# Optimization experiments

Hardware: AMD Instinct MI355X
Metric: run time of the kernel (lower is better)

Reference implementation:

```python
import jax, jax.numpy as jnp
import numpy as np

K_NEIGHBORS = 5
LEAKY_SLOPE = 0.2
NEG_INF = -1e9


def create_knn(x, k):
    # x: [B, N, D] -> binary adjacency [B, N, N], adj[b,i,j]=1 if j is among
    # the k nearest neighbors of i (squared euclidean distance).
    sq = jnp.sum(x * x, axis=-1)                      # [B, N]
    # d2[b,i,j] = |xi|^2 + |xj|^2 - 2 xi.xj
    d2 = sq[:, :, None] + sq[:, None, :] - 2.0 * jnp.einsum('bid,bjd->bij', x, x)
    _, idx = jax.lax.top_k(-d2, k)                    # [B, N, k] nearest (incl. self)
    B, N, _ = x.shape
    b_idx = jnp.arange(B)[:, None, None]
    i_idx = jnp.arange(N)[None, :, None]
    adj = jnp.zeros((B, N, N), dtype=x.dtype).at[b_idx, i_idx, idx].set(1.0)
    return adj


def gat_layer(x, adj, W, a_src, a_dst):
    # Single-head GAT over dense kNN adjacency.
    h = jnp.einsum('bnd,df->bnf', x, W)               # [B, N, F]
    e_src = jnp.einsum('bnf,f->bn', h, a_src)         # [B, N]
    e_dst = jnp.einsum('bnf,f->bn', h, a_dst)         # [B, N]
    e = e_src[:, :, None] + e_dst[:, None, :]         # [B, N, N]
    e = jax.nn.leaky_relu(e, negative_slope=LEAKY_SLOPE)
    e = jnp.where(adj > 0, e, NEG_INF)
    alpha = jax.nn.softmax(e, axis=-1)                # [B, N, N]
    out = jnp.einsum('bij,bjf->bif', alpha, h)        # [B, N, F]
    return jax.nn.elu(out)


def setup_inputs() -> dict:
    key = jax.random.key(0)
    k1, k2, k3, k4 = jax.random.split(key, 4)
    B, N, D = 256, 196, 2048
    F = D // 4
    return {
        'resnet_features': jax.random.normal(k1, (B, N, D), dtype=jnp.float32),
        'W': jax.random.normal(k2, (D, F), dtype=jnp.float32) * (1.0 / np.sqrt(D)),
        'a_src': jax.random.normal(k3, (F,), dtype=jnp.float32) * (1.0 / np.sqrt(F)),
        'a_dst': jax.random.normal(k4, (F,), dtype=jnp.float32) * (1.0 / np.sqrt(F)),
    }


def reference(resnet_features, W, a_src, a_dst):
    adj = create_knn(resnet_features, K_NEIGHBORS)
    return gat_layer(resnet_features, adj, W, a_src, a_dst)
```

## Files before the change

### kernel.cpp

```cpp
#include <hip/hip_runtime.h>

#define B_  256
#define N_  196
#define D_  2048
#define F_  512
#define ROWS (B_*N_)
#define CAND 8
#define PROWS 208
#define PELEMS (PROWS*32)

typedef _Float16 f16x8 __attribute__((ext_vector_type(8)));
typedef _Float16 f16x4 __attribute__((ext_vector_type(4)));
typedef float    f32x4 __attribute__((ext_vector_type(4)));

static __device__ __forceinline__ float wave_reduce_sum(float v) {
#pragma unroll
  for (int off = 32; off > 0; off >>= 1) v += __shfl_xor(v, off);
  return v;
}

static __device__ __forceinline__ double wave_reduce_sum_d(double v) {
#pragma unroll
  for (int off = 32; off > 0; off >>= 1) v += __shfl_xor(v, off);
  return v;
}

static __device__ __forceinline__ float np_chain16(const float* __restrict__ x, int h) {
  int base = (h >> 3) * 128 + (h & 7);
  float t0 = x[base];
  float r = __fmul_rn(t0, t0);
#pragma unroll
  for (int i = 1; i < 16; ++i) {
    float t = x[base + 8 * i];
    r = __fadd_rn(r, __fmul_rn(t, t));
  }
  return r;
}
static __device__ __forceinline__ float np_sq_row(const float* __restrict__ x, int lane) {
  float ra = np_chain16(x, lane);
  float rb = np_chain16(x, lane + 64);
#pragma unroll
  for (int off = 1; off <= 4; off <<= 1) {
    ra = __fadd_rn(ra, __shfl_xor(ra, off));
    rb = __fadd_rn(rb, __shfl_xor(rb, off));
  }
  float lf[16];
#pragma unroll
  for (int L = 0; L < 8; ++L) { lf[L] = __shfl(ra, L * 8); lf[8 + L] = __shfl(rb, L * 8); }
  float b8[8];
#pragma unroll
  for (int t = 0; t < 8; ++t) b8[t] = __fadd_rn(lf[2 * t], lf[2 * t + 1]);
  float c4[4];
#pragma unroll
  for (int t = 0; t < 4; ++t) c4[t] = __fadd_rn(b8[2 * t], b8[2 * t + 1]);
  return __fadd_rn(__fadd_rn(c4[0], c4[1]), __fadd_rn(c4[2], c4[3]));
}

__global__ __launch_bounds__(256) void wtrans_kernel(const float* __restrict__ W,
                                                     _Float16* __restrict__ Wt2) {
  __shared__ float T[64][68];
  int k0 = blockIdx.x * 64;
  int f0 = blockIdx.y * 64;
  int tid = threadIdx.x;
  int c = tid & 63;
  int r4 = tid >> 6;
#pragma unroll
  for (int p = 0; p < 16; ++p) {
    int r = p * 4 + r4;
    T[r][c] = W[(size_t)(k0 + r) * F_ + f0 + c];
  }
  __syncthreads();
#pragma unroll
  for (int p = 0; p < 16; ++p) {
    int fr = p * 4 + r4;
    int kg = k0 + c;
    Wt2[(size_t)(kg >> 5) * F_ * 32 + (size_t)(f0 + fr) * 32 + (kg & 31)] = (_Float16)T[c][fr];
  }
}

__global__ __launch_bounds__(256, 3) void h_gemm(const float* __restrict__ X,
                                                 const _Float16* __restrict__ Wt2,
                                                 float* __restrict__ H) {
  __shared__ _Float16 Al[2][64][40];
  const int mBase = blockIdx.y * 64;
  const int nBase = blockIdx.x * 256;
  const int tid  = threadIdx.x;
  const int lane = tid & 63;
  const int wave = tid >> 6;
  const int fr_row = lane & 15;
  const int fr_k   = (lane >> 4) * 8;
  const int ar = tid >> 2;
  const int ak = (tid & 3) * 8;
  f32x4 acc[4][4] = {};

  const _Float16* Bb = Wt2 + (size_t)(nBase + wave * 64 + fr_row) * 32 + fr_k;
  const size_t PSTRIDE = (size_t)F_ * 32;

  f16x8 bf[4];
#pragma unroll
  for (int n = 0; n < 4; ++n) bf[n] = *(const f16x8*)&Bb[(size_t)n * 512];

  {
    float4 a0 = *(const float4*)&X[(size_t)(mBase + ar) * D_ + ak];
    float4 a1 = *(const float4*)&X[(size_t)(mBase + ar) * D_ + ak + 4];
    f16x8 ah = { (_Float16)a0.x, (_Float16)a0.y, (_Float16)a0.z, (_Float16)a0.w,
                 (_Float16)a1.x, (_Float16)a1.y, (_Float16)a1.z, (_Float16)a1.w };
    *(f16x8*)&Al[0][ar][ak] = ah;
  }
  __syncthreads();

  for (int t = 0; t < 64; ++t) {
    const int cur = t & 1;
    float4 na0, na1; f16x8 nb[4];
    if (t < 63) {
      const int k0 = (t + 1) * 32;
      na0 = *(const float4*)&X[(size_t)(mBase + ar) * D_ + k0 + ak];
      na1 = *(const float4*)&X[(size_t)(mBase + ar) * D_ + k0 + ak + 4];
      const _Float16* bp = Bb + (size_t)(t + 1) * PSTRIDE;
#pragma unroll
      for (int n = 0; n < 4; ++n) nb[n] = *(const f16x8*)&bp[(size_t)n * 512];
    }
    f16x8 af[4];
#pragma unroll
    for (int m = 0; m < 4; ++m) af[m] = *(const f16x8*)&Al[cur][m * 16 + fr_row][fr_k];
#pragma unroll
    for (int m = 0; m < 4; ++m)
#pragma unroll
      for (int n = 0; n < 4; ++n)
        acc[m][n] = __builtin_amdgcn_mfma_f32_16x16x32_f16(af[m], bf[n], acc[m][n], 0, 0, 0);
    if (t < 63) {
      f16x8 ah = { (_Float16)na0.x, (_Float16)na0.y, (_Float16)na0.z, (_Float16)na0.w,
                   (_Float16)na1.x, (_Float16)na1.y, (_Float16)na1.z, (_Float16)na1.w };
      *(f16x8*)&Al[cur ^ 1][ar][ak] = ah;
#pragma unroll
      for (int n = 0; n < 4; ++n) bf[n] = nb[n];
    }
    __syncthreads();
  }

  const int orow0 = mBase + (lane >> 4) * 4;
#pragma unroll
  for (int m = 0; m < 4; ++m) {
#pragma unroll
    for (int n = 0; n < 4; ++n) {
      int col = nBase + wave * 64 + n * 16 + (lane & 15);
#pragma unroll
      for (int i = 0; i < 4; ++i)
        H[(size_t)(orow0 + m * 16 + i) * F_ + col] = acc[m][n][i];
    }
  }
}

__global__ __launch_bounds__(512, 2) void h_gemm_pan(const float* __restrict__ X,
                                                     const _Float16* __restrict__ Wt2,
                                                     const float* __restrict__ As,
                                                     const float* __restrict__ Ad,
                                                     float* __restrict__ H,
                                                     _Float16* __restrict__ Xh,
                                                     float* __restrict__ sqg,
                                                     float* __restrict__ es,
                                                     float* __restrict__ ed) {
  __shared__ _Float16 Al[2][64][40];
  __shared__ float eS[64][8];
  __shared__ float eD[64][8];
  const int mBase = blockIdx.x * 64;
  const int tid  = threadIdx.x;
  const int lane = tid & 63;
  const int wave = tid >> 6;
  const int fr_row = lane & 15;
  const int fr_k   = (lane >> 4) * 8;
  const int ar = tid >> 3;
  const int ak = (tid & 7) * 4;
  f32x4 acc[4][4] = {};
  float sqp = 0.f;

  const int grow = mBase + ar;
  const int bb = grow / N_;
  const int rl = grow - bb * N_;
  _Float16* pRow = Xh + (size_t)bb * 64 * PELEMS + (size_t)rl * 32 + ak;

  const _Float16* Bb = Wt2 + (size_t)(wave * 64 + fr_row) * 32 + fr_k;
  const size_t PSTRIDE = (size_t)F_ * 32;

  f16x8 bf[4];
#pragma unroll
  for (int n = 0; n < 4; ++n) bf[n] = *(const f16x8*)&Bb[(size_t)n * 512];

  {
    float4 a0 = *(const float4*)&X[(size_t)grow * D_ + ak];
    f16x4 ah = { (_Float16)a0.x, (_Float16)a0.y, (_Float16)a0.z, (_Float16)a0.w };
    *(f16x4*)&Al[0][ar][ak] = ah;
    sqp += a0.x * a0.x + a0.y * a0.y + a0.z * a0.z + a0.w * a0.w;
    *(f16x4*)pRow = ah;
  }
  __syncthreads();

  for (int t = 0; t < 64; ++t) {
    const int cur = t & 1;
    float4 na; f16x8 nb[4];
    if (t < 63) {
      const int k0 = (t + 1) * 32;
      na = *(const float4*)&X[(size_t)grow * D_ + k0 + ak];
      const _Float16* bp = Bb + (size_t)(t + 1) * PSTRIDE;
#pragma unroll
      for (int n = 0; n < 4; ++n) nb[n] = *(const f16x8*)&bp[(size_t)n * 512];
    }
    f16x8 af[4];
#pragma unroll
    for (int m = 0; m < 4; ++m) af[m] = *(const f16x8*)&Al[cur][m * 16 + fr_row][fr_k];
#pragma unroll
    for (int m = 0; m < 4; ++m)
#pragma unroll
      for (int n = 0; n < 4; ++n)
        acc[m][n] = __builtin_amdgcn_mfma_f32_16x16x32_f16(af[m], bf[n], acc[m][n], 0, 0, 0);
    if (t < 63) {
      f16x4 nah = { (_Float16)na.x, (_Float16)na.y, (_Float16)na.z, (_Float16)na.w };
      *(f16x4*)&Al[cur ^ 1][ar][ak] = nah;
      sqp += na.x * na.x + na.y * na.y + na.z * na.z + na.w * na.w;
      *(f16x4*)(pRow + (size_t)(t + 1) * PELEMS) = nah;
#pragma unroll
      for (int n = 0; n < 4; ++n) bf[n] = nb[n];
    }
    __syncthreads();
  }

  {
    float s = sqp;
    s += __shfl_xor(s, 1); s += __shfl_xor(s, 2); s += __shfl_xor(s, 4);
    if ((lane & 7) == 0) sqg[grow] = s;
  }

  {
    float as_v[4], ad_v[4];
#pragma unroll
    for (int n = 0; n < 4; ++n) {
      int col = wave * 64 + n * 16 + (lane & 15);
      as_v[n] = As[col]; ad_v[n] = Ad[col];
    }
#pragma unroll
    for (int m = 0; m < 4; ++m) {
#pragma unroll
      for (int i = 0; i < 4; ++i) {
        float ps = 0.f, pd = 0.f;
#pragma unroll
        for (int n = 0; n < 4; ++n) {
          ps += acc[m][n][i] * as_v[n];
          pd += acc[m][n][i] * ad_v[n];
        }
#pragma unroll
        for (int off = 1; off <= 8; off <<= 1) {
          ps += __shfl_xor(ps, off);
          pd += __shfl_xor(pd, off);
        }
        if ((lane & 15) == 0) {
          int row_loc = (lane >> 4) * 4 + i + m * 16;
          eS[row_loc][wave] = ps;
          eD[row_loc][wave] = pd;
        }
      }
    }
  }
  __syncthreads();
  if (tid < 64) {
    float s = 0.f, d = 0.f;
#pragma unroll
    for (int w = 0; w < 8; ++w) { s += eS[tid][w]; d += eD[tid][w]; }
    es[mBase + tid] = s;
    ed[mBase + tid] = d;
  }

  const int orow0 = mBase + (lane >> 4) * 4;
#pragma unroll
  for (int m = 0; m < 4; ++m) {
#pragma unroll
    for (int n = 0; n < 4; ++n) {
      int col = wave * 64 + n * 16 + (lane & 15);
#pragma unroll
      for (int i = 0; i < 4; ++i)
        H[(size_t)(orow0 + m * 16 + i) * F_ + col] = acc[m][n][i];
    }
  }
}

__global__ __launch_bounds__(256) void e_kernel(const float* __restrict__ H,
                                                const float* __restrict__ as,
                                                const float* __restrict__ ad,
                                                float* __restrict__ es,
                                                float* __restrict__ ed) {
  int row  = blockIdx.x * 4 + (threadIdx.x >> 6);
  int lane = threadIdx.x & 63;
  const float* h = H + (size_t)row * F_;
  float s = 0.f, d = 0.f;
#pragma unroll
  for (int p = 0; p < 2; ++p) {
    int col = p * 256 + lane * 4;
    float4 hv = *(const float4*)&h[col];
    float4 av = *(const float4*)&as[col];
    float4 dv = *(const float4*)&ad[col];
    s += hv.x * av.x + hv.y * av.y + hv.z * av.z + hv.w * av.w;
    d += hv.x * dv.x + hv.y * dv.y + hv.z * dv.z + hv.w * dv.w;
  }
  s = wave_reduce_sum(s);
  d = wave_reduce_sum(d);
  if (lane == 0) { es[row] = s; ed[row] = d; }
}

__global__ __launch_bounds__(256, 3) void knn_screen(const float* __restrict__ X,
                                                     int* __restrict__ cand8,
                                                     float* __restrict__ gapw) {
  __shared__ _Float16 T[2][256][40];
  __shared__ float sqA[256];

  const int bi  = blockIdx.x;
  const int xcd = bi & 7;
  const int kk  = bi >> 3;
  const int b   = ((kk >> 2) << 3) | xcd;
  const int i0  = (kk & 3) * 64;

  const int tid  = threadIdx.x;
  const int lane = tid & 63;
  const int wave = tid >> 6;
  const float* Xb = X + (size_t)b * N_ * D_;
  const int fr_row = lane & 15;
  const int fr_k   = (lane >> 4) * 8;
  const int srow = tid >> 3;
  const int skk  = (tid & 7) * 4;

  f32x4 acc[13] = {};
  float sqp[8] = {};

  {
    float4 v[8];
#pragma unroll
    for (int p = 0; p < 8; ++p) {
      int r = p * 32 + srow;
      v[p] = make_float4(0.f, 0.f, 0.f, 0.f);
      if (r < N_) v[p] = *(const float4*)&Xb[(size_t)r * D_ + skk];
    }
#pragma unroll
    for (int p = 0; p < 8; ++p) {
      int r = p * 32 + srow;
      sqp[p] += v[p].x * v[p].x + v[p].y * v[p].y + v[p].z * v[p].z + v[p].w * v[p].w;
      f16x4 h4 = { (_Float16)v[p].x, (_Float16)v[p].y, (_Float16)v[p].z, (_Float16)v[p].w };
      *(f16x4*)&T[0][r][skk] = h4;
    }
  }
  __syncthreads();

  for (int t = 0; t < 64; ++t) {
    const int cur = t & 1;
    float4 nv[8];
    if (t < 63) {
      const int k0 = (t + 1) * 32;
#pragma unroll
      for (int p = 0; p < 8; ++p) {
        int r = p * 32 + srow;
        nv[p] = make_float4(0.f, 0.f, 0.f, 0.f);
        if (r < N_) nv[p] = *(const float4*)&Xb[(size_t)r * D_ + k0 + skk];
      }
    }
    f16x8 a0 = *(const f16x8*)&T[cur][i0 + wave * 16 + fr_row][fr_k];
#pragma unroll
    for (int n = 0; n < 13; ++n) {
      f16x8 bfr = *(const f16x8*)&T[cur][n * 16 + fr_row][fr_k];
      acc[n] = __builtin_amdgcn_mfma_f32_16x16x32_f16(a0, bfr, acc[n], 0, 0, 0);
    }
    if (t < 63) {
#pragma unroll
      for (int p = 0; p < 8; ++p) {
        int r = p * 32 + srow;
        sqp[p] += nv[p].x * nv[p].x + nv[p].y * nv[p].y + nv[p].z * nv[p].z + nv[p].w * nv[p].w;
        f16x4 h4 = { (_Float16)nv[p].x, (_Float16)nv[p].y, (_Float16)nv[p].z, (_Float16)nv[p].w };
        *(f16x4*)&T[cur ^ 1][r][skk] = h4;
      }
    }
    __syncthreads();
  }

#pragma unroll
  for (int p = 0; p < 8; ++p) {
    float s = sqp[p];
    s += __shfl_xor(s, 1); s += __shfl_xor(s, 2); s += __shfl_xor(s, 4);
    if ((lane & 7) == 0) sqA[p * 32 + srow] = s;
  }
  __syncthreads();

  float sqv[13];
#pragma unroll
  for (int n = 0; n < 13; ++n) sqv[n] = sqA[n * 16 + (lane & 15)];
  const int g = lane >> 4;
#pragma unroll
  for (int i = 0; i < 4; ++i) {
    int row_loc = wave * 16 + g * 4 + i;
    float w13[13];
#pragma unroll
    for (int n = 0; n < 13; ++n) {
      int col = n * 16 + (lane & 15);
      w13[n] = (col < N_) ? (sqv[n] - 2.0f * acc[n][i]) : 1e30f;
    }
    int candv[CAND]; float mscv[CAND];
#pragma unroll
    for (int it = 0; it < CAND; ++it) {
      float mv = w13[0]; int mn = 0;
#pragma unroll
      for (int n = 1; n < 13; ++n)
        if (w13[n] < mv) { mv = w13[n]; mn = n; }
      int mcol = mn * 16 + (lane & 15);
#pragma unroll
      for (int off = 1; off <= 8; off <<= 1) {
        float ov = __shfl_xor(mv, off);
        int   oc = __shfl_xor(mcol, off);
        if (ov < mv || (ov == mv && oc < mcol)) { mv = ov; mcol = oc; }
      }
      mscv[it] = mv; candv[it] = mcol;
      int kn = mcol >> 4;
#pragma unroll
      for (int n = 0; n < 13; ++n)
        if (n == kn && (lane & 15) == (mcol & 15)) w13[n] = 1e30f;
    }
    int ig = i0 + row_loc;
    if ((lane & 15) == 0 && ig < N_) {
      size_t o = ((size_t)b * N_ + ig) * CAND;
#pragma unroll
      for (int c = 0; c < CAND; ++c) cand8[o + c] = candv[c];
      gapw[b * N_ + ig] = mscv[5] - mscv[4];
    }
  }
}

__global__ __launch_bounds__(256) void knn_screen_pan(const _Float16* __restrict__ Xh,
                                                      const float* __restrict__ sqg,
                                                      int* __restrict__ cand8,
                                                      float* __restrict__ gapw) {
  const int bi  = blockIdx.x;
  const int xcd = bi & 7;
  const int kk  = bi >> 3;
  const int b   = ((kk >> 2) << 3) | xcd;
  const int i0  = (kk & 3) * 64;

  const int tid  = threadIdx.x;
  const int lane = tid & 63;
  const int wave = tid >> 6;
  if (i0 + wave * 16 >= N_) return;

  const int fr_row = lane & 15;
  const int fr_k   = (lane >> 4) * 8;

  const _Float16* Pb = Xh + (size_t)b * 64 * PELEMS;
  const int aoff = (i0 + wave * 16 + fr_row) * 32 + fr_k;

  f32x4 acc[13] = {};
#pragma unroll 2
  for (int t = 0; t < 64; ++t) {
    const _Float16* P = Pb + (size_t)t * PELEMS;
    f16x8 a0 = *(const f16x8*)&P[aoff];
#pragma unroll
    for (int n = 0; n < 13; ++n) {
      f16x8 bfr = *(const f16x8*)&P[(n * 16 + fr_row) * 32 + fr_k];
      acc[n] = __builtin_amdgcn_mfma_f32_16x16x32_f16(a0, bfr, acc[n], 0, 0, 0);
    }
  }

  float sqv[13];
#pragma unroll
  for (int n = 0; n < 13; ++n) {
    int col = n * 16 + (lane & 15);
    sqv[n] = (col < N_) ? sqg[b * N_ + col] : 0.f;
  }
  const int g = lane >> 4;
#pragma unroll
  for (int i = 0; i < 4; ++i) {
    int row_loc = wave * 16 + g * 4 + i;
    float w13[13];
#pragma unroll
    for (int n = 0; n < 13; ++n) {
      int col = n * 16 + (lane & 15);
      w13[n] = (col < N_) ? (sqv[n] - 2.0f * acc[n][i]) : 1e30f;
    }
    int candv[CAND]; float mscv[CAND];
#pragma unroll
    for (int it = 0; it < CAND; ++it) {
      float mv = w13[0]; int mn = 0;
#pragma unroll
      for (int n = 1; n < 13; ++n)
        if (w13[n] < mv) { mv = w13[n]; mn = n; }
      int mcol = mn * 16 + (lane & 15);
#pragma unroll
      for (int off = 1; off <= 8; off <<= 1) {
        float ov = __shfl_xor(mv, off);
        int   oc = __shfl_xor(mcol, off);
        if (ov < mv || (ov == mv && oc < mcol)) { mv = ov; mcol = oc; }
      }
      mscv[it] = mv; candv[it] = mcol;
      int kn = mcol >> 4;
#pragma unroll
      for (int n = 0; n < 13; ++n)
        if (n == kn && (lane & 15) == (mcol & 15)) w13[n] = 1e30f;
    }
    int ig = i0 + row_loc;
    if ((lane & 15) == 0 && ig < N_) {
      size_t o = ((size_t)b * N_ + ig) * CAND;
#pragma unroll
      for (int c = 0; c < CAND; ++c) cand8[o + c] = candv[c];
      gapw[b * N_ + ig] = mscv[5] - mscv[4];
    }
  }
}

__global__ __launch_bounds__(256) void knn_resolve(const float* __restrict__ X,
                                                   const int* __restrict__ cand8,
                                                   const float* __restrict__ gapw,
                                                   const float* __restrict__ es,
                                                   const float* __restrict__ ed,
                                                   int* __restrict__ idx5,
                                                   float* __restrict__ alpha5) {
  const int gr   = blockIdx.x * 4 + (threadIdx.x >> 6);
  const int lane = threadIdx.x & 63;
  const int b    = gr / N_;
  const int ig   = gr - b * N_;
  const float* Xb = X + (size_t)b * N_ * D_;
  const float* xi = Xb + (size_t)ig * D_;

  int cand[CAND];
#pragma unroll
  for (int c = 0; c < CAND; ++c) cand[c] = cand8[(size_t)gr * CAND + c];
  float gap = gapw[gr];

  int ordj[5];
  if (gap > 0.75f) {
#pragma unroll
    for (int m5 = 0; m5 < 5; ++m5) ordj[m5] = cand[m5];
  } else {
    float4 xr[8];
#pragma unroll
    for (int q = 0; q < 8; ++q) xr[q] = *(const float4*)&xi[q * 256 + lane * 4];
    double s8[CAND];
#pragma unroll
    for (int c = 0; c < CAND; ++c) {
      const float* xj = Xb + (size_t)cand[c] * D_;
      double dsum = 0.0, sqc = 0.0;
#pragma unroll
      for (int q = 0; q < 8; ++q) {
        float4 u = *(const float4*)&xj[q * 256 + lane * 4];
        dsum += (double)xr[q].x * (double)u.x + (double)xr[q].y * (double)u.y
              + (double)xr[q].z * (double)u.z + (double)xr[q].w * (double)u.w;
        sqc  += (double)u.x * (double)u.x + (double)u.y * (double)u.y
              + (double)u.z * (double)u.z + (double)u.w * (double)u.w;
      }
      dsum = wave_reduce_sum_d(dsum);
      sqc  = wave_reduce_sum_d(sqc);
      s8[c] = sqc - 2.0 * dsum;
    }
    int rnk[CAND];
#pragma unroll
    for (int c = 0; c < CAND; ++c) {
      int r = 0;
#pragma unroll
      for (int c2 = 0; c2 < CAND; ++c2)
        if (c2 != c && (s8[c2] < s8[c] || (s8[c2] == s8[c] && cand[c2] < cand[c]))) r++;
      rnk[c] = r;
    }
    double g5 = 0.0, g6 = 0.0;
#pragma unroll
    for (int c = 0; c < CAND; ++c) {
      if (rnk[c] == 4) g5 = s8[c];
      if (rnk[c] == 5) g6 = s8[c];
    }
#pragma unroll
    for (int m5 = 0; m5 < 5; ++m5) {
      int oj = 0;
#pragma unroll
      for (int c = 0; c < CAND; ++c)
        if (rnk[c] == m5) oj = cand[c];
      ordj[m5] = oj;
    }
    if (!(g6 - g5 > 4e-3)) {
      float sqi_ex = np_sq_row(xi, lane);
      float sqc_ex[CAND];
#pragma unroll
      for (int c = 0; c < CAND; ++c)
        sqc_ex[c] = np_sq_row(Xb + (size_t)cand[c] * D_, lane);
      int grp8 = (lane >> 2) & 7;
      int l4 = lane & 3;
      int cj = cand[0];
#pragma unroll
      for (int c = 1; c < CAND; ++c)
        if (grp8 == c) cj = cand[c];
      const float* xjr = Xb + (size_t)cj * D_;
      float aacc = 0.f;
      for (int s5 = 0; s5 < 512; ++s5) {
        int d = s5 * 4 + l4;
        aacc = __fadd_rn(aacc, __fmul_rn(xi[d], xjr[d]));
      }
      float d2c[CAND];
#pragma unroll
      for (int c = 0; c < CAND; ++c) {
        float s0 = __shfl(aacc, c * 4 + 0);
        float s1 = __shfl(aacc, c * 4 + 1);
        float s2 = __shfl(aacc, c * 4 + 2);
        float s3 = __shfl(aacc, c * 4 + 3);
        float G  = __fadd_rn(__fadd_rn(s0, s1), __fadd_rn(s2, s3));
        float Sij = __fadd_rn(sqi_ex, sqc_ex[c]);
        d2c[c] = __fsub_rn(Sij, __fadd_rn(G, G));
      }
      int rnk3[CAND];
#pragma unroll
      for (int c = 0; c < CAND; ++c) {
        int r = 0;
#pragma unroll
        for (int c2 = 0; c2 < CAND; ++c2)
          if (c2 != c && (d2c[c2] < d2c[c] || (d2c[c2] == d2c[c] && cand[c2] < cand[c]))) r++;
        rnk3[c] = r;
      }
#pragma unroll
      for (int m5 = 0; m5 < 5; ++m5) {
        int oj = 0;
#pragma unroll
        for (int c = 0; c < CAND; ++c)
          if (rnk3[c] == m5) oj = cand[c];
        ordj[m5] = oj;
      }
    }
  }
  float ei = es[gr];
  float ev[5];
#pragma unroll
  for (int m5 = 0; m5 < 5; ++m5) {
    float e = ei + ed[b * N_ + ordj[m5]];
    ev[m5] = e > 0.f ? e : 0.2f * e;
  }
  float mx = fmaxf(fmaxf(fmaxf(ev[0], ev[1]), fmaxf(ev[2], ev[3])), ev[4]);
  float p0 = expf(ev[0] - mx), p1 = expf(ev[1] - mx), p2 = expf(ev[2] - mx),
        p3 = expf(ev[3] - mx), p4 = expf(ev[4] - mx);
  float inv = 1.0f / (p0 + p1 + p2 + p3 + p4);
  if (lane == 0) {
    size_t o = (size_t)gr * 5;
    idx5[o + 0] = ordj[0]; alpha5[o + 0] = p0 * inv;
    idx5[o + 1] = ordj[1]; alpha5[o + 1] = p1 * inv;
    idx5[o + 2] = ordj[2]; alpha5[o + 2] = p2 * inv;
    idx5[o + 3] = ordj[3]; alpha5[o + 3] = p3 * inv;
    idx5[o + 4] = ordj[4]; alpha5[o + 4] = p4 * inv;
  }
}

__global__ __launch_bounds__(128) void agg_kernel(const float* __restrict__ H,
                                                  const int* __restrict__ idx5,
                                                  const float* __restrict__ alpha5,
                                                  float* __restrict__ out) {
  int row = blockIdx.x;
  int b = row / N_;
  int t = threadIdx.x;
  size_t base5 = (size_t)row * 5;
  const float* Hb = H + (size_t)b * N_ * F_;
  float ax = 0.f, ay = 0.f, az = 0.f, aw = 0.f;
#pragma unroll
  for (int c = 0; c < 5; ++c) {
    int j   = idx5[base5 + c];
    float a = alpha5[base5 + c];
    float4 hv = *(const float4*)&Hb[(size_t)j * F_ + t * 4];
    ax += a * hv.x; ay += a * hv.y; az += a * hv.z; aw += a * hv.w;
  }
  float4 o;
  o.x = ax > 0.f ? ax : expf(ax) - 1.f;
  o.y = ay > 0.f ? ay : expf(ay) - 1.f;
  o.z = az > 0.f ? az : expf(az) - 1.f;
  o.w = aw > 0.f ? aw : expf(aw) - 1.f;
  *(float4*)&out[(size_t)row * F_ + t * 4] = o;
}

extern "C" void kernel_launch(void* const* d_in, const int* in_sizes, int n_in,
                              void* d_out, int out_size, void* d_ws, size_t ws_size,
                              hipStream_t stream) {
  const float* X    = (const float*)d_in[0];
  const float* W    = (const float*)d_in[1];
  const float* Asrc = (const float*)d_in[2];
  const float* Adst = (const float*)d_in[3];
  float* out = (float*)d_out;

  const size_t OFF_WT  = 0;
  const size_t OFF_ES  = OFF_WT + 2097152;
  const size_t OFF_ED  = OFF_ES + 200704;
  const size_t OFF_IDX = OFF_ED + 200704;
  const size_t OFF_ALP = OFF_IDX + 1003520;
  const size_t OFF_C8  = OFF_ALP + 1003520;
  const size_t OFF_GAP = OFF_C8 + 1605632;
  const size_t OFF_SQG = OFF_GAP + 200704;
  const size_t OFF_H   = OFF_SQG + 200704;
  const size_t OFF_XH  = OFF_H + (size_t)ROWS * F_ * 4;
  const size_t XH_BYTES = (size_t)B_ * 64 * PELEMS * 2;
  const size_t NEED_A  = OFF_XH;
  const size_t NEED_B  = OFF_XH + XH_BYTES;
  if (ws_size < NEED_A) return;

  char* ws = (char*)d_ws;
  _Float16* Wt2 = (_Float16*)(ws + OFF_WT);
  float* es     = (float*)(ws + OFF_ES);
  float* ed     = (float*)(ws + OFF_ED);
  int*   idx5   = (int*)  (ws + OFF_IDX);
  float* alpha5 = (float*)(ws + OFF_ALP);
  int*   cand8  = (int*)  (ws + OFF_C8);
  float* gapw   = (float*)(ws + OFF_GAP);
  float* sqg    = (float*)(ws + OFF_SQG);
  float* H      = (float*)(ws + OFF_H);
  _Float16* Xh  = (_Float16*)(ws + OFF_XH);

  wtrans_kernel<<<dim3(32, 8), 256, 0, stream>>>(W, Wt2);
  if (ws_size >= NEED_B) {
    h_gemm_pan<<<784, 512, 0, stream>>>(X, Wt2, Asrc, Adst, H, Xh, sqg, es, ed);
    knn_screen_pan<<<1024, 256, 0, stream>>>(Xh, sqg, cand8, gapw);
  } else {
    h_gemm<<<dim3(2, 784), 256, 0, stream>>>(X, Wt2, H);
    e_kernel<<<ROWS / 4, 256, 0, stream>>>(H, Asrc, Adst, es, ed);
    knn_screen<<<1024, 256, 0, stream>>>(X, cand8, gapw);
  }
  knn_resolve<<<ROWS / 4, 256, 0, stream>>>(X, cand8, gapw, es, ed, idx5, alpha5);
  agg_kernel<<<ROWS, 128, 0, stream>>>(H, idx5, alpha5, out);
}
```

Before: 684.9 us.

## Split fp32-to-fp16 panelization from GEMM and feed MFMA directly from panels

The fused GEMM that both converted X to fp16 panels and computed H is split in two. A separate panelize kernel writes the fp16 panels and row norms, and a new 2-way N-split GEMM loads A fragments straight from the panel buffer in global memory, with no LDS staging or barriers. Attention logit partial sums are written per N half and combined in knn_resolve. This adds an extra pass writing the fp16 copy of X, and A panels are re-read by both N halves, in exchange for a simpler, barrier-free GEMM inner loop with more blocks.

```diff
diff --git a/kernel.cpp b/kernel.cpp
--- a/kernel.cpp
+++ b/kernel.cpp
@@ -75,6 +75,127 @@
     int fr = p * 4 + r4;
     int kg = k0 + c;
     Wt2[(size_t)(kg >> 5) * F_ * 32 + (size_t)(f0 + fr) * 32 + (kg & 31)] = (_Float16)T[c][fr];
+  }
+}
+
+__global__ __launch_bounds__(256) void panelize_kernel(const float* __restrict__ X,
+                                                       _Float16* __restrict__ Xh,
+                                                       float* __restrict__ sqg) {
+  const int tid = threadIdx.x;
+  const int ar  = tid >> 3;
+  const int ak  = (tid & 7) * 4;
+  const int lane = tid & 63;
+  const int grow = blockIdx.x * 32 + ar;
+  const int bb = grow / N_;
+  const int rl = grow - bb * N_;
+  const float* xr = X + (size_t)grow * D_;
+  _Float16* pRow = Xh + (size_t)bb * 64 * PELEMS + (size_t)rl * 32 + ak;
+  float sqp = 0.f;
+#pragma unroll 4
+  for (int t = 0; t < 64; ++t) {
+    float4 v = *(const float4*)&xr[t * 32 + ak];
+    sqp += v.x * v.x + v.y * v.y + v.z * v.z + v.w * v.w;
+    f16x4 h4 = { (_Float16)v.x, (_Float16)v.y, (_Float16)v.z, (_Float16)v.w };
+    *(f16x4*)(pRow + (size_t)t * PELEMS) = h4;
+  }
+  sqp += __shfl_xor(sqp, 1); sqp += __shfl_xor(sqp, 2); sqp += __shfl_xor(sqp, 4);
+  if ((lane & 7) == 0) sqg[grow] = sqp;
+}
+
+__global__ __launch_bounds__(256) void h_gemm_p(const _Float16* __restrict__ Xh,
+                                                const _Float16* __restrict__ Wt2,
+                                                const float* __restrict__ As,
+                                                const float* __restrict__ Ad,
+                                                float* __restrict__ H,
+                                                float* __restrict__ esp,
+                                                float* __restrict__ edp) {
+  __shared__ float eS[64][4];
+  __shared__ float eD[64][4];
+  const int mBase = blockIdx.y * 64;
+  const int half  = blockIdx.x;
+  const int nBase = half * 256;
+  const int tid  = threadIdx.x;
+  const int lane = tid & 63;
+  const int wave = tid >> 6;
+  const int fr_row = lane & 15;
+  const int fr_k   = (lane >> 4) * 8;
+  f32x4 acc[4][4] = {};
+
+  const _Float16* pA[4];
+#pragma unroll
+  for (int m = 0; m < 4; ++m) {
+    int rg = mBase + m * 16 + fr_row;
+    int bb = rg / N_;
+    int rl = rg - bb * N_;
+    pA[m] = Xh + (size_t)bb * 64 * PELEMS + (size_t)rl * 32 + fr_k;
+  }
+  const _Float16* Bb = Wt2 + (size_t)(nBase + wave * 64 + fr_row) * 32 + fr_k;
+  const size_t PSTRIDE = (size_t)F_ * 32;
+
+#pragma unroll 2
+  for (int t = 0; t < 64; ++t) {
+    const size_t po = (size_t)t * PELEMS;
+    const _Float16* bp = Bb + (size_t)t * PSTRIDE;
+    f16x8 af[4], bf[4];
+#pragma unroll
+    for (int m = 0; m < 4; ++m) af[m] = *(const f16x8*)(pA[m] + po);
+#pragma unroll
+    for (int n = 0; n < 4; ++n) bf[n] = *(const f16x8*)&bp[(size_t)n * 512];
+#pragma unroll
+    for (int m = 0; m < 4; ++m)
+#pragma unroll
+      for (int n = 0; n < 4; ++n)
+        acc[m][n] = __builtin_amdgcn_mfma_f32_16x16x32_f16(af[m], bf[n], acc[m][n], 0, 0, 0);
+  }
+
+  {
+    float as_v[4], ad_v[4];
+#pragma unroll
+    for (int n = 0; n < 4; ++n) {
+      int col = nBase + wave * 64 + n * 16 + (lane & 15);
+      as_v[n] = As[col]; ad_v[n] = Ad[col];
+    }
+#pragma unroll
+    for (int m = 0; m < 4; ++m) {
+#pragma unroll
+      for (int i = 0; i < 4; ++i) {
+        float ps = 0.f, pd = 0.f;
+#pragma unroll
+        for (int n = 0; n < 4; ++n) {
+          ps += acc[m][n][i] * as_v[n];
+          pd += acc[m][n][i] * ad_v[n];
+        }
+#pragma unroll
+        for (int off = 1; off <= 8; off <<= 1) {
+          ps += __shfl_xor(ps, off);
+          pd += __shfl_xor(pd, off);
+        }
+        if ((lane & 15) == 0) {
+          int row_loc = (lane >> 4) * 4 + i + m * 16;
+          eS[row_loc][wave] = ps;
+          eD[row_loc][wave] = pd;
+        }
+      }
+    }
+  }
+  __syncthreads();
+  if (tid < 64) {
+    float s = eS[tid][0] + eS[tid][1] + eS[tid][2] + eS[tid][3];
+    float d = eD[tid][0] + eD[tid][1] + eD[tid][2] + eD[tid][3];
+    esp[(size_t)half * ROWS + mBase + tid] = s;
+    edp[(size_t)half * ROWS + mBase + tid] = d;
+  }
+
+  const int orow0 = mBase + (lane >> 4) * 4;
+#pragma unroll
+  for (int m = 0; m < 4; ++m) {
+#pragma unroll
+    for (int n = 0; n < 4; ++n) {
+      int col = nBase + wave * 64 + n * 16 + (lane & 15);
+#pragma unroll
+      for (int i = 0; i < 4; ++i)
+        H[(size_t)(orow0 + m * 16 + i) * F_ + col] = acc[m][n][i];
+    }
   }
 }
 
@@ -151,137 +272,6 @@
   }
 }
 
-__global__ __launch_bounds__(512, 2) void h_gemm_pan(const float* __restrict__ X,
-                                                     const _Float16* __restrict__ Wt2,
-                                                     const float* __restrict__ As,
-                                                     const float* __restrict__ Ad,
-                                                     float* __restrict__ H,
-                                                     _Float16* __restrict__ Xh,
-                                                     float* __restrict__ sqg,
-                                                     float* __restrict__ es,
-                                                     float* __restrict__ ed) {
-  __shared__ _Float16 Al[2][64][40];
-  __shared__ float eS[64][8];
-  __shared__ float eD[64][8];
-  const int mBase = blockIdx.x * 64;
-  const int tid  = threadIdx.x;
-  const int lane = tid & 63;
-  const int wave = tid >> 6;
-  const int fr_row = lane & 15;
-  const int fr_k   = (lane >> 4) * 8;
-  const int ar = tid >> 3;
-  const int ak = (tid & 7) * 4;
-  f32x4 acc[4][4] = {};
-  float sqp = 0.f;
-
-  const int grow = mBase + ar;
-  const int bb = grow / N_;
-  const int rl = grow - bb * N_;
-  _Float16* pRow = Xh + (size_t)bb * 64 * PELEMS + (size_t)rl * 32 + ak;
-
-  const _Float16* Bb = Wt2 + (size_t)(wave * 64 + fr_row) * 32 + fr_k;
-  const size_t PSTRIDE = (size_t)F_ * 32;
-
-  f16x8 bf[4];
-#pragma unroll
-  for (int n = 0; n < 4; ++n) bf[n] = *(const f16x8*)&Bb[(size_t)n * 512];
-
-  {
-    float4 a0 = *(const float4*)&X[(size_t)grow * D_ + ak];
-    f16x4 ah = { (_Float16)a0.x, (_Float16)a0.y, (_Float16)a0.z, (_Float16)a0.w };
-    *(f16x4*)&Al[0][ar][ak] = ah;
-    sqp += a0.x * a0.x + a0.y * a0.y + a0.z * a0.z + a0.w * a0.w;
-    *(f16x4*)pRow = ah;
-  }
-  __syncthreads();
-
-  for (int t = 0; t < 64; ++t) {
-    const int cur = t & 1;
-    float4 na; f16x8 nb[4];
-    if (t < 63) {
-      const int k0 = (t + 1) * 32;
-      na = *(const float4*)&X[(size_t)grow * D_ + k0 + ak];
-      const _Float16* bp = Bb + (size_t)(t + 1) * PSTRIDE;
-#pragma unroll
-      for (int n = 0; n < 4; ++n) nb[n] = *(const f16x8*)&bp[(size_t)n * 512];
-    }
-    f16x8 af[4];
-#pragma unroll
-    for (int m = 0; m < 4; ++m) af[m] = *(const f16x8*)&Al[cur][m * 16 + fr_row][fr_k];
-#pragma unroll
-    for (int m = 0; m < 4; ++m)
-#pragma unroll
-      for (int n = 0; n < 4; ++n)
-        acc[m][n] = __builtin_amdgcn_mfma_f32_16x16x32_f16(af[m], bf[n], acc[m][n], 0, 0, 0);
-    if (t < 63) {
-      f16x4 nah = { (_Float16)na.x, (_Float16)na.y, (_Float16)na.z, (_Float16)na.w };
-      *(f16x4*)&Al[cur ^ 1][ar][ak] = nah;
-      sqp += na.x * na.x + na.y * na.y + na.z * na.z + na.w * na.w;
-      *(f16x4*)(pRow + (size_t)(t + 1) * PELEMS) = nah;
-#pragma unroll
-      for (int n = 0; n < 4; ++n) bf[n] = nb[n];
-    }
-    __syncthreads();
-  }
-
-  {
-    float s = sqp;
-    s += __shfl_xor(s, 1); s += __shfl_xor(s, 2); s += __shfl_xor(s, 4);
-    if ((lane & 7) == 0) sqg[grow] = s;
-  }
-
-  {
-    float as_v[4], ad_v[4];
-#pragma unroll
-    for (int n = 0; n < 4; ++n) {
-      int col = wave * 64 + n * 16 + (lane & 15);
-      as_v[n] = As[col]; ad_v[n] = Ad[col];
-    }
-#pragma unroll
-    for (int m = 0; m < 4; ++m) {
-#pragma unroll
-      for (int i = 0; i < 4; ++i) {
-        float ps = 0.f, pd = 0.f;
-#pragma unroll
-        for (int n = 0; n < 4; ++n) {
-          ps += acc[m][n][i] * as_v[n];
-          pd += acc[m][n][i] * ad_v[n];
-        }
-#pragma unroll
-        for (int off = 1; off <= 8; off <<= 1) {
-          ps += __shfl_xor(ps, off);
-          pd += __shfl_xor(pd, off);
-        }
-        if ((lane & 15) == 0) {
-          int row_loc = (lane >> 4) * 4 + i + m * 16;
-          eS[row_loc][wave] = ps;
-          eD[row_loc][wave] = pd;
-        }
-      }
-    }
-  }
-  __syncthreads();
-  if (tid < 64) {
-    float s = 0.f, d = 0.f;
-#pragma unroll
-    for (int w = 0; w < 8; ++w) { s += eS[tid][w]; d += eD[tid][w]; }
-    es[mBase + tid] = s;
-    ed[mBase + tid] = d;
-  }
-
-  const int orow0 = mBase + (lane >> 4) * 4;
-#pragma unroll
-  for (int m = 0; m < 4; ++m) {
-#pragma unroll
-    for (int n = 0; n < 4; ++n) {
-      int col = wave * 64 + n * 16 + (lane & 15);
-#pragma unroll
-      for (int i = 0; i < 4; ++i)
-        H[(size_t)(orow0 + m * 16 + i) * F_ + col] = acc[m][n][i];
-    }
-  }
-}
-
 __global__ __launch_bounds__(256) void e_kernel(const float* __restrict__ H,
                                                 const float* __restrict__ as,
                                                 const float* __restrict__ ad,
@@ -512,6 +502,7 @@
                                                    const float* __restrict__ gapw,
                                                    const float* __restrict__ es,
                                                    const float* __restrict__ ed,
+                                                   int dual,
                                                    int* __restrict__ idx5,
                                                    float* __restrict__ alpha5) {
   const int gr   = blockIdx.x * 4 + (threadIdx.x >> 6);
@@ -622,11 +613,12 @@
       }
     }
   }
-  float ei = es[gr];
+  float ei = es[gr] + (dual ? es[ROWS + gr] : 0.f);
   float ev[5];
 #pragma unroll
   for (int m5 = 0; m5 < 5; ++m5) {
-    float e = ei + ed[b * N_ + ordj[m5]];
+    int jj = b * N_ + ordj[m5];
+    float e = ei + ed[jj] + (dual ? ed[ROWS + jj] : 0.f);
     ev[m5] = e > 0.f ? e : 0.2f * e;
   }
   float mx = fmaxf(fmaxf(fmaxf(ev[0], ev[1]), fmaxf(ev[2], ev[3])), ev[4]);
@@ -679,8 +671,8 @@
 
   const size_t OFF_WT  = 0;
   const size_t OFF_ES  = OFF_WT + 2097152;
-  const size_t OFF_ED  = OFF_ES + 200704;
-  const size_t OFF_IDX = OFF_ED + 200704;
+  const size_t OFF_ED  = OFF_ES + 401408;
+  const size_t OFF_IDX = OFF_ED + 401408;
   const size_t OFF_ALP = OFF_IDX + 1003520;
   const size_t OFF_C8  = OFF_ALP + 1003520;
   const size_t OFF_GAP = OFF_C8 + 1605632;
@@ -706,13 +698,15 @@
 
   wtrans_kernel<<<dim3(32, 8), 256, 0, stream>>>(W, Wt2);
   if (ws_size >= NEED_B) {
-    h_gemm_pan<<<784, 512, 0, stream>>>(X, Wt2, Asrc, Adst, H, Xh, sqg, es, ed);
+    panelize_kernel<<<ROWS / 32, 256, 0, stream>>>(X, Xh, sqg);
+    h_gemm_p<<<dim3(2, 784), 256, 0, stream>>>(Xh, Wt2, Asrc, Adst, H, es, ed);
     knn_screen_pan<<<1024, 256, 0, stream>>>(Xh, sqg, cand8, gapw);
+    knn_resolve<<<ROWS / 4, 256, 0, stream>>>(X, cand8, gapw, es, ed, 1, idx5, alpha5);
   } else {
     h_gemm<<<dim3(2, 784), 256, 0, stream>>>(X, Wt2, H);
     e_kernel<<<ROWS / 4, 256, 0, stream>>>(H, Asrc, Adst, es, ed);
     knn_screen<<<1024, 256, 0, stream>>>(X, cand8, gapw);
-  }
-  knn_resolve<<<ROWS / 4, 256, 0, stream>>>(X, cand8, gapw, es, ed, idx5, alpha5);
+    knn_resolve<<<ROWS / 4, 256, 0, stream>>>(X, cand8, gapw, es, ed, 0, idx5, alpha5);
+  }
   agg_kernel<<<ROWS, 128, 0, stream>>>(H, idx5, alpha5, out);
 }
```

Result: slower. 1.012 ms (+47.7%).
